# Optimization experiments

Measured on AMD Instinct MI355X. Metric: run time of the kernel, lower is better.

Reference implementation:

```python
import jax, jax.numpy as jnp
import numpy as np

NUM_HEADS = 16

def setup_inputs() -> dict:
    key = jax.random.key(0)
    k1, k2, k3, k4 = jax.random.split(key, 4)
    B, N, C = 4, 2048, 1024
    x = jax.random.normal(k1, (B, N, C), dtype=jnp.float32)
    xpos = jax.random.randint(k2, (B, N), 0, 2048, dtype=jnp.int64)
    Wqkv = jax.random.normal(k3, (C, 3 * C), dtype=jnp.float32) * (C ** -0.5)
    Wproj = jax.random.normal(k4, (C, C), dtype=jnp.float32) * (C ** -0.5)
    bproj = jnp.zeros((C,), dtype=jnp.float32)
    return {"x": x, "xpos": xpos, "Wqkv": Wqkv, "Wproj": Wproj, "bproj": bproj}

def reference(x, xpos, Wqkv, Wproj, bproj):
    # rope is None in this configuration, so xpos is unused (matches torch default path).
    B, N, C = x.shape
    H = NUM_HEADS
    Dh = C // H
    scale = Dh ** -0.5
    qkv = jnp.einsum('bnc,cd->bnd', x, Wqkv)              # [B, N, 3C]
    qkv = qkv.reshape(B, N, 3, H, Dh)
    q, k, v = qkv[:, :, 0], qkv[:, :, 1], qkv[:, :, 2]    # [B, N, H, Dh]
    scores = jnp.einsum('bnhd,bmhd->bhnm', q, k) * scale  # [B, H, N, N]
    attn = jax.nn.softmax(scores, axis=-1)
    out = jnp.einsum('bhnm,bmhd->bnhd', attn, v)          # [B, N, H, Dh]
    out = out.reshape(B, N, C)
    return jnp.einsum('bnc,cd->bnd', out, Wproj) + bproj
```

## Files before the change

kernel.cpp:

```cpp
#include <hip/hip_runtime.h>
#include <stdint.h>

#define DEVINL __device__ __forceinline__

typedef __bf16 bf16x8 __attribute__((ext_vector_type(8)));
typedef float f32x4 __attribute__((ext_vector_type(4)));
typedef float f32x16 __attribute__((ext_vector_type(16)));
typedef uint32_t u32x4 __attribute__((ext_vector_type(4)));

DEVINL uint16_t f2bf(float f) {
    uint32_t u = __builtin_bit_cast(uint32_t, f);
    uint32_t r = (u + 0x7FFFu + ((u >> 16) & 1u)) >> 16;
    return (uint16_t)r;
}

DEVINL bf16x8 ld8(const uint16_t* p) {
    u32x4 v = *(const u32x4*)p;
    return __builtin_bit_cast(bf16x8, v);
}

DEVINL void gload16(const void* g, void* l) {
    __builtin_amdgcn_global_load_lds(
        (const __attribute__((address_space(1))) uint32_t*)g,
        (__attribute__((address_space(3))) uint32_t*)l, 16, 0, 0);
}

DEVINL uint32_t cvtpk(float lo, float hi) {
    uint32_t r;
    asm("v_cvt_pk_bf16_f32 %0, %1, %2" : "=v"(r) : "v"(lo), "v"(hi));
    return r;
}

DEVINL float exp2_fast(float x) {
    float r;
    asm("v_exp_f32 %0, %1" : "=v"(r) : "v"(x));
    return r;
}

DEVINL void transW_body(const float* __restrict__ W, uint16_t* __restrict__ WT,
                        int Nn, int n0, int k0, int tid, uint16_t* t) {
#pragma unroll
    for (int i = 0; i < 4; ++i) {
        int c = tid + i * 256;
        int kr = c >> 4, nc = c & 15;
        float4 v = *(const float4*)(W + (size_t)(k0 + kr) * Nn + n0 + nc * 4);
        t[(nc * 4 + 0) * 65 + kr] = f2bf(v.x);
        t[(nc * 4 + 1) * 65 + kr] = f2bf(v.y);
        t[(nc * 4 + 2) * 65 + kr] = f2bf(v.z);
        t[(nc * 4 + 3) * 65 + kr] = f2bf(v.w);
    }
    __syncthreads();
#pragma unroll
    for (int i = 0; i < 2; ++i) {
        int c = tid + i * 256;
        int nr = c >> 3, kc = c & 7;
        union { uint16_t u[8]; u32x4 v; } o;
#pragma unroll
        for (int j = 0; j < 8; ++j) o.u[j] = t[nr * 65 + kc * 8 + j];
        *(u32x4*)(WT + (size_t)(n0 + nr) * 1024 + k0 + kc * 8) = o.v;
    }
}

__global__ void k_prep(const float* __restrict__ x, uint16_t* __restrict__ xb,
                       const float* __restrict__ Wqkv, uint16_t* __restrict__ wqkvT,
                       const float* __restrict__ Wproj, uint16_t* __restrict__ wprojT) {
    __shared__ uint16_t t[64 * 65];
    int bid = blockIdx.x;
    int tid = threadIdx.x;
    if (bid < 4096) {
        int i = bid * 256 + tid;
        const float4* src = (const float4*)x + (size_t)i * 2;
        float4 a = src[0], b = src[1];
        union { uint16_t u[8]; u32x4 v; } o;
        o.u[0] = f2bf(a.x); o.u[1] = f2bf(a.y); o.u[2] = f2bf(a.z); o.u[3] = f2bf(a.w);
        o.u[4] = f2bf(b.x); o.u[5] = f2bf(b.y); o.u[6] = f2bf(b.z); o.u[7] = f2bf(b.w);
        ((u32x4*)xb)[i] = o.v;
    } else if (bid < 4864) {
        int idx = bid - 4096;
        transW_body(Wqkv, wqkvT, 3072, (idx % 48) * 64, (idx / 48) * 64, tid, t);
    } else {
        int idx = bid - 4864;
        transW_body(Wproj, wprojT, 1024, (idx % 16) * 64, (idx / 16) * 64, tid, t);
    }
}

template <int MODE>
__global__ __launch_bounds__(256) void k_gemm(
    const uint16_t* __restrict__ A, const uint16_t* __restrict__ BT,
    const float* __restrict__ bias,
    uint16_t* __restrict__ qo, uint16_t* __restrict__ ko, uint16_t* __restrict__ vo,
    float* __restrict__ out) {
    __shared__ uint16_t smem[16640];
    uint16_t* a_lds = smem;
    uint16_t* b_lds = smem + 8192;
    int tid = threadIdx.x;
    int w = tid >> 6, l = tid & 63;
    int l15 = l & 15, l4 = l >> 4;
    int bid = blockIdx.x;
    int mt = ((bid & 7) << 3) + ((bid >> 3) & 7);
    int nt = bid >> 6;
    int m0 = mt * 128, n0 = nt * 128;
    int wr = w >> 1, wc = w & 1;
    f32x4 acc[4][4] = {};

    for (int kt = 0; kt < 16; ++kt) {
#pragma unroll
        for (int i = 0; i < 4; ++i) {
            int c = i * 256 + w * 64 + l;
            int row = c >> 3, slot = c & 7;
            int kc = slot ^ (row & 7);
            gload16(A + (size_t)(m0 + row) * 1024 + kt * 64 + kc * 8,
                    a_lds + (size_t)(i * 256 + w * 64) * 8);
            gload16(BT + (size_t)(n0 + row) * 1024 + kt * 64 + kc * 8,
                    b_lds + (size_t)(i * 256 + w * 64) * 8);
        }
        __syncthreads();
#pragma unroll
        for (int kkk = 0; kkk < 2; ++kkk) {
            bf16x8 af[4], bfr[4];
#pragma unroll
            for (int i = 0; i < 4; ++i) {
                int row = wr * 64 + i * 16 + l15;
                af[i] = ld8(a_lds + row * 64 + ((kkk * 4 + l4) ^ (row & 7)) * 8);
                int rowb = wc * 64 + i * 16 + l15;
                bfr[i] = ld8(b_lds + rowb * 64 + ((kkk * 4 + l4) ^ (rowb & 7)) * 8);
            }
#pragma unroll
            for (int i = 0; i < 4; ++i)
#pragma unroll
                for (int j = 0; j < 4; ++j)
                    acc[i][j] = __builtin_amdgcn_mfma_f32_16x16x32_bf16(
                        af[i], bfr[j], acc[i][j], 0, 0, 0);
        }
        __syncthreads();
    }

    if constexpr (MODE == 0) {
        if (n0 >= 2048) {
#pragma unroll
            for (int i = 0; i < 4; ++i)
#pragma unroll
                for (int j = 0; j < 4; ++j) {
                    int dl = wc * 64 + j * 16 + l15;
                    int ml = wr * 64 + i * 16 + l4 * 4;
                    union { uint16_t u[4]; uint2 v2; } pk;
#pragma unroll
                    for (int r = 0; r < 4; ++r) pk.u[r] = f2bf(acc[i][j][r]);
                    *(uint2*)&smem[dl * 130 + ml] = pk.v2;
                }
            __syncthreads();
            int b = m0 >> 11, nbase = m0 & 2047;
#pragma unroll
            for (int pass = 0; pass < 8; ++pass) {
                int dl = pass * 16 + (tid >> 4);
                int mloc = (tid & 15) * 8;
                u32x4 val = *(u32x4*)&smem[dl * 130 + mloc];
                int d = n0 + dl;
                int h = (d >> 6) & 15, dh = d & 63;
                *(u32x4*)(vo + ((size_t)(b * 16 + h) * 64 + dh) * 2048 + nbase + mloc) = val;
            }
        } else {
#pragma unroll
            for (int i = 0; i < 4; ++i)
#pragma unroll
                for (int j = 0; j < 4; ++j) {
                    int d = n0 + wc * 64 + j * 16 + l15;
                    int s = d >> 10, h = (d >> 6) & 15, dh = d & 63;
                    uint16_t* dst0 = (s == 0) ? qo : ko;
                    float sc = (s == 0) ? 0.18033688011112042f : 1.0f;
#pragma unroll
                    for (int r = 0; r < 4; ++r) {
                        int m = m0 + wr * 64 + i * 16 + l4 * 4 + r;
                        int b = m >> 11, n = m & 2047;
                        dst0[((size_t)(b * 16 + h) * 2048 + n) * 64 + dh] = f2bf(acc[i][j][r] * sc);
                    }
                }
        }
    } else {
#pragma unroll
        for (int j = 0; j < 4; ++j) {
            int d = n0 + wc * 64 + j * 16 + l15;
            float bv = bias[d];
#pragma unroll
            for (int i = 0; i < 4; ++i)
#pragma unroll
                for (int r = 0; r < 4; ++r) {
                    int m = m0 + wr * 64 + i * 16 + l4 * 4 + r;
                    out[(size_t)m * 1024 + d] = acc[i][j][r] + bv;
                }
        }
    }
}

__global__ __launch_bounds__(256) void k_attn(
    const uint16_t* __restrict__ q, const uint16_t* __restrict__ kk_,
    const uint16_t* __restrict__ vt, uint16_t* __restrict__ o) {
    __shared__ uint16_t k_lds[2][64 * 64];
    __shared__ uint16_t v_lds[2][64 * 64];
    int tid = threadIdx.x;
    int w = tid >> 6, l = tid & 63;
    int l31 = l & 31, g = l >> 5;
    int bid = blockIdx.x;
    int slot = bid >> 3;
    int bh = (bid & 7) * 8 + (slot >> 4);
    int qt = slot & 15;
    int qrow = qt * 128 + w * 32 + l31;
    const uint16_t* qb = q + ((size_t)bh * 2048 + qrow) * 64;
    const uint16_t* kbase = kk_ + (size_t)bh * 2048 * 64;
    const uint16_t* vbase = vt + (size_t)bh * 64 * 2048;

    bf16x8 qf[4];
#pragma unroll
    for (int kv = 0; kv < 4; ++kv) qf[kv] = ld8(qb + kv * 16 + g * 8);

    int c0 = w * 128 + l;
    int rr0 = c0 >> 3, sl0 = c0 & 7;
    int kc0 = sl0 ^ (rr0 & 7);
    int rr1 = rr0 + 8, kc1 = sl0 ^ (rr1 & 7);
    const uint16_t* kp0 = kbase + rr0 * 64 + kc0 * 8;
    const uint16_t* kp1 = kbase + rr1 * 64 + kc1 * 8;
    const uint16_t* vp0 = vbase + (size_t)rr0 * 2048 + kc0 * 8;
    const uint16_t* vp1 = vbase + (size_t)rr1 * 2048 + kc1 * 8;
    uint16_t* kd0 = k_lds[0] + w * 1024;
    uint16_t* kd1 = k_lds[1] + w * 1024;
    uint16_t* vd0 = v_lds[0] + w * 1024;
    uint16_t* vd1 = v_lds[1] + w * 1024;

    f32x16 oa[2] = {};
    float lsum = 0.f;

    auto stage = [&](uint16_t* kd, uint16_t* vd) {
        gload16(kp0, kd);       gload16(kp1, kd + 512);
        gload16(vp0, vd);       gload16(vp1, vd + 512);
        kp0 += 4096; kp1 += 4096; vp0 += 64; vp1 += 64;
    };

    stage(kd0, vd0);

    auto body = [&](int t, const uint16_t* kb, const uint16_t* vb,
                    uint16_t* kdn, uint16_t* vdn) {
        asm volatile("s_waitcnt vmcnt(2)\n\ts_barrier" ::: "memory");
        if (t < 31) stage(kdn, vdn);

        bf16x8 pfrag[4];
#pragma unroll
        for (int j = 0; j < 2; ++j) {
            int key = j * 32 + l31;
            f32x16 stj = {};
            __builtin_amdgcn_s_setprio(1);
#pragma unroll
            for (int kv = 0; kv < 4; ++kv) {
                bf16x8 kf = ld8(kb + key * 64 + ((2 * kv + g) ^ (key & 7)) * 8);
                stj = __builtin_amdgcn_mfma_f32_32x32x16_bf16(kf, qf[kv], stj, 0, 0, 0);
            }
            __builtin_amdgcn_s_setprio(0);
#pragma unroll
            for (int h = 0; h < 2; ++h) {
                float e[8];
#pragma unroll
                for (int jj = 0; jj < 8; ++jj) e[jj] = exp2_fast(stj[h * 8 + jj]);
                lsum += ((e[0] + e[1]) + (e[2] + e[3])) + ((e[4] + e[5]) + (e[6] + e[7]));
                uint32_t a0 = cvtpk(e[0], e[1]), a1 = cvtpk(e[2], e[3]);
                uint32_t b0 = cvtpk(e[4], e[5]), b1 = cvtpk(e[6], e[7]);
                auto r0 = __builtin_amdgcn_permlane32_swap(a0, b0, false, false);
                auto r1 = __builtin_amdgcn_permlane32_swap(a1, b1, false, false);
                u32x4 f;
                f[0] = r0[0]; f[1] = r1[0]; f[2] = r0[1]; f[3] = r1[1];
                pfrag[j * 2 + h] = __builtin_bit_cast(bf16x8, f);
            }
        }

        if (t < 31) asm volatile("s_waitcnt vmcnt(4)\n\ts_barrier" ::: "memory");
        else        asm volatile("s_waitcnt vmcnt(0)\n\ts_barrier" ::: "memory");

        __builtin_amdgcn_s_setprio(1);
#pragma unroll
        for (int kv = 0; kv < 4; ++kv) {
#pragma unroll
            for (int dt = 0; dt < 2; ++dt) {
                int dh = dt * 32 + l31;
                bf16x8 vf = ld8(vb + dh * 64 + ((2 * kv + g) ^ (dh & 7)) * 8);
                oa[dt] = __builtin_amdgcn_mfma_f32_32x32x16_bf16(vf, pfrag[kv], oa[dt], 0, 0, 0);
            }
        }
        __builtin_amdgcn_s_setprio(0);
    };

    for (int kt = 0; kt < 32; kt += 2) {
        body(kt,     k_lds[0], v_lds[0], kd1, vd1);
        body(kt + 1, k_lds[1], v_lds[1], kd0, vd0);
    }

    float ltot = lsum + __shfl_xor(lsum, 32, 64);
    float inv = 1.0f / ltot;
    int b = bh >> 4, h = bh & 15;
    uint16_t* ob = o + ((size_t)(b * 2048 + qrow)) * 1024 + h * 64;
#pragma unroll
    for (int dt = 0; dt < 2; ++dt)
#pragma unroll
        for (int rq = 0; rq < 4; ++rq) {
            union { uint16_t u[4]; uint2 v; } pk;
#pragma unroll
            for (int rr = 0; rr < 4; ++rr) pk.u[rr] = f2bf(oa[dt][rq * 4 + rr] * inv);
            int dh0 = dt * 32 + rq * 8 + g * 4;
            *(uint2*)(ob + dh0) = pk.v;
        }
}

extern "C" void kernel_launch(void* const* d_in, const int* in_sizes, int n_in,
                              void* d_out, int out_size, void* d_ws, size_t ws_size,
                              hipStream_t stream) {
    const float* x     = (const float*)d_in[0];
    const float* Wqkv  = (const float*)d_in[2];
    const float* Wproj = (const float*)d_in[3];
    const float* bproj = (const float*)d_in[4];
    float* out = (float*)d_out;

    char* ws = (char*)d_ws;
    uint16_t* xb     = (uint16_t*)(ws);
    uint16_t* wqkvT  = (uint16_t*)(ws + 16777216);
    uint16_t* wprojT = (uint16_t*)(ws + 23068672);
    uint16_t* qws    = (uint16_t*)(ws + 25165824);
    uint16_t* kws    = (uint16_t*)(ws + 41943040);
    uint16_t* vT     = (uint16_t*)(ws + 58720256);
    uint16_t* attnout = xb;

    k_prep<<<dim3(5120), dim3(256), 0, stream>>>(x, xb, Wqkv, wqkvT, Wproj, wprojT);
    k_gemm<0><<<dim3(1536), dim3(256), 0, stream>>>(xb, wqkvT, nullptr, qws, kws, vT, nullptr);
    k_attn<<<dim3(1024), dim3(256), 0, stream>>>(qws, kws, vT, attnout);
    k_gemm<1><<<dim3(512), dim3(256), 0, stream>>>(attnout, wprojT, bproj, nullptr, nullptr, nullptr, out);
}
```

Measured before the change: 204.4 us.

## Restructure GEMM to 256x128 tiles, 512 threads, double-buffered LDS pipeline

Rewrites the bf16 GEMM kernel to use 256x128 output tiles with 8 waves, double-buffered LDS staging through global_load_lds so the next K-slice loads while the current one computes, and s_setprio around the MFMA bursts. Grid sizes are halved and 96KB of dynamic LDS is requested. The aim is to hide global load latency and raise arithmetic intensity per block. In exchange, the large LDS footprint and 512-thread blocks reduce occupancy, and the 256-block projection GEMM may underfill the GPU's compute units.

```diff
diff --git a/kernel.cpp b/kernel.cpp
--- a/kernel.cpp
+++ b/kernel.cpp
@@ -85,108 +85,124 @@
 }
 
 template <int MODE>
-__global__ __launch_bounds__(256) void k_gemm(
+__global__ __launch_bounds__(512) void k_gemm(
     const uint16_t* __restrict__ A, const uint16_t* __restrict__ BT,
     const float* __restrict__ bias,
     uint16_t* __restrict__ qo, uint16_t* __restrict__ ko, uint16_t* __restrict__ vo,
     float* __restrict__ out) {
-    __shared__ uint16_t smem[16640];
-    uint16_t* a_lds = smem;
-    uint16_t* b_lds = smem + 8192;
+    extern __shared__ uint16_t lds[];
     int tid = threadIdx.x;
     int w = tid >> 6, l = tid & 63;
     int l15 = l & 15, l4 = l >> 4;
+    int wr = w >> 2, wc = w & 3;
     int bid = blockIdx.x;
-    int mt = ((bid & 7) << 3) + ((bid >> 3) & 7);
-    int nt = bid >> 6;
-    int m0 = mt * 128, n0 = nt * 128;
-    int wr = w >> 1, wc = w & 1;
-    f32x4 acc[4][4] = {};
-
-    for (int kt = 0; kt < 16; ++kt) {
-#pragma unroll
-        for (int i = 0; i < 4; ++i) {
-            int c = i * 256 + w * 64 + l;
-            int row = c >> 3, slot = c & 7;
-            int kc = slot ^ (row & 7);
-            gload16(A + (size_t)(m0 + row) * 1024 + kt * 64 + kc * 8,
-                    a_lds + (size_t)(i * 256 + w * 64) * 8);
-            gload16(BT + (size_t)(n0 + row) * 1024 + kt * 64 + kc * 8,
-                    b_lds + (size_t)(i * 256 + w * 64) * 8);
-        }
+    int mt = (bid & 7) * 4 + ((bid >> 3) & 3);
+    int nt = bid >> 5;
+    int m0 = mt * 256, n0 = nt * 128;
+
+    int r0 = tid >> 3, sl0 = tid & 7;
+    int kc = sl0 ^ (r0 & 7);
+    const uint16_t* pA = A + (size_t)(m0 + r0) * 1024 + kc * 8;
+    const uint16_t* pB = BT + (size_t)(n0 + r0) * 1024 + kc * 8;
+    int wofs = w * 512;
+
+    f32x4 acc[8][2] = {};
+
+    auto stageK = [&](int ks, int abA, int abB) {
+#pragma unroll
+        for (int q = 0; q < 4; ++q)
+            gload16(pA + q * 65536 + ks * 64, lds + abA + q * 4096 + wofs);
+#pragma unroll
+        for (int li = 0; li < 2; ++li)
+            gload16(pB + li * 65536 + ks * 64, lds + abB + li * 4096 + wofs);
+    };
+
+    auto computeK = [&](int abA, int abB) {
+        const uint16_t* Ah = lds + abA + wr * 8192;
+        const uint16_t* Bb = lds + abB;
+#pragma unroll
+        for (int kk = 0; kk < 2; ++kk) {
+            int ch = ((kk * 4 + l4) ^ (l15 & 7)) * 8;
+            bf16x8 af[8], bf[2];
+#pragma unroll
+            for (int fi = 0; fi < 8; ++fi)
+                af[fi] = ld8(Ah + (fi * 16 + l15) * 64 + ch);
+#pragma unroll
+            for (int fj = 0; fj < 2; ++fj)
+                bf[fj] = ld8(Bb + (wc * 32 + fj * 16 + l15) * 64 + ch);
+            __builtin_amdgcn_s_setprio(1);
+#pragma unroll
+            for (int fi = 0; fi < 8; ++fi)
+#pragma unroll
+                for (int fj = 0; fj < 2; ++fj)
+                    acc[fi][fj] = __builtin_amdgcn_mfma_f32_16x16x32_bf16(
+                        af[fi], bf[fj], acc[fi][fj], 0, 0, 0);
+            __builtin_amdgcn_s_setprio(0);
+        }
+    };
+
+    stageK(0, 0, 32768);
+    asm volatile("s_waitcnt vmcnt(0)\n\ts_barrier" ::: "memory");
+    for (int s = 0; s < 16; s += 2) {
+        if (s + 1 < 16) stageK(s + 1, 16384, 40960);
+        computeK(0, 32768);
+        asm volatile("s_waitcnt vmcnt(0)\n\ts_barrier" ::: "memory");
+        if (s + 2 < 16) stageK(s + 2, 0, 32768);
+        computeK(16384, 40960);
+        asm volatile("s_waitcnt vmcnt(0)\n\ts_barrier" ::: "memory");
+    }
+
+    if constexpr (MODE == 0) {
+        int b = m0 >> 11, nbase = m0 & 2047;
+        if (n0 >= 2048) {
+#pragma unroll
+            for (int fi = 0; fi < 8; ++fi)
+#pragma unroll
+                for (int fj = 0; fj < 2; ++fj) {
+                    int dl = wc * 32 + fj * 16 + l15;
+                    int ml = wr * 128 + fi * 16 + l4 * 4;
+                    union { uint16_t u[4]; uint2 v2; } pk;
+#pragma unroll
+                    for (int r = 0; r < 4; ++r) pk.u[r] = f2bf(acc[fi][fj][r]);
+                    *(uint2*)&lds[dl * 264 + ml] = pk.v2;
+                }
         __syncthreads();
 #pragma unroll
-        for (int kkk = 0; kkk < 2; ++kkk) {
-            bf16x8 af[4], bfr[4];
-#pragma unroll
-            for (int i = 0; i < 4; ++i) {
-                int row = wr * 64 + i * 16 + l15;
-                af[i] = ld8(a_lds + row * 64 + ((kkk * 4 + l4) ^ (row & 7)) * 8);
-                int rowb = wc * 64 + i * 16 + l15;
-                bfr[i] = ld8(b_lds + rowb * 64 + ((kkk * 4 + l4) ^ (rowb & 7)) * 8);
-            }
-#pragma unroll
-            for (int i = 0; i < 4; ++i)
-#pragma unroll
-                for (int j = 0; j < 4; ++j)
-                    acc[i][j] = __builtin_amdgcn_mfma_f32_16x16x32_bf16(
-                        af[i], bfr[j], acc[i][j], 0, 0, 0);
-        }
-        __syncthreads();
-    }
-
-    if constexpr (MODE == 0) {
-        if (n0 >= 2048) {
-#pragma unroll
-            for (int i = 0; i < 4; ++i)
-#pragma unroll
-                for (int j = 0; j < 4; ++j) {
-                    int dl = wc * 64 + j * 16 + l15;
-                    int ml = wr * 64 + i * 16 + l4 * 4;
-                    union { uint16_t u[4]; uint2 v2; } pk;
-#pragma unroll
-                    for (int r = 0; r < 4; ++r) pk.u[r] = f2bf(acc[i][j][r]);
-                    *(uint2*)&smem[dl * 130 + ml] = pk.v2;
-                }
-            __syncthreads();
-            int b = m0 >> 11, nbase = m0 & 2047;
-#pragma unroll
-            for (int pass = 0; pass < 8; ++pass) {
-                int dl = pass * 16 + (tid >> 4);
-                int mloc = (tid & 15) * 8;
-                u32x4 val = *(u32x4*)&smem[dl * 130 + mloc];
-                int d = n0 + dl;
-                int h = (d >> 6) & 15, dh = d & 63;
-                *(u32x4*)(vo + ((size_t)(b * 16 + h) * 64 + dh) * 2048 + nbase + mloc) = val;
+            for (int it = 0; it < 8; ++it) {
+                int idx = it * 512 + tid;
+                int row = idx >> 5, col = (idx & 31) * 8;
+                u32x4 val = *(u32x4*)&lds[row * 264 + col];
+                int dv = (n0 - 2048) + row;
+                int h = dv >> 6, dh = dv & 63;
+                *(u32x4*)(vo + ((size_t)(b * 16 + h) * 64 + dh) * 2048 + nbase + col) = val;
             }
         } else {
-#pragma unroll
-            for (int i = 0; i < 4; ++i)
-#pragma unroll
-                for (int j = 0; j < 4; ++j) {
-                    int d = n0 + wc * 64 + j * 16 + l15;
-                    int s = d >> 10, h = (d >> 6) & 15, dh = d & 63;
-                    uint16_t* dst0 = (s == 0) ? qo : ko;
-                    float sc = (s == 0) ? 0.18033688011112042f : 1.0f;
+            float sc = (n0 < 1024) ? 0.18033688011112042f : 1.0f;
+            uint16_t* dst0 = (n0 < 1024) ? qo : ko;
+#pragma unroll
+            for (int fi = 0; fi < 8; ++fi)
+#pragma unroll
+                for (int fj = 0; fj < 2; ++fj) {
+                    int d = n0 + wc * 32 + fj * 16 + l15;
+                    int h = (d >> 6) & 15, dh = d & 63;
 #pragma unroll
                     for (int r = 0; r < 4; ++r) {
-                        int m = m0 + wr * 64 + i * 16 + l4 * 4 + r;
-                        int b = m >> 11, n = m & 2047;
-                        dst0[((size_t)(b * 16 + h) * 2048 + n) * 64 + dh] = f2bf(acc[i][j][r] * sc);
+                        int n = nbase + wr * 128 + fi * 16 + l4 * 4 + r;
+                        dst0[((size_t)(b * 16 + h) * 2048 + n) * 64 + dh] = f2bf(acc[fi][fj][r] * sc);
                     }
                 }
         }
     } else {
 #pragma unroll
-        for (int j = 0; j < 4; ++j) {
-            int d = n0 + wc * 64 + j * 16 + l15;
+        for (int fj = 0; fj < 2; ++fj) {
+            int d = n0 + wc * 32 + fj * 16 + l15;
             float bv = bias[d];
 #pragma unroll
-            for (int i = 0; i < 4; ++i)
+            for (int fi = 0; fi < 8; ++fi)
 #pragma unroll
                 for (int r = 0; r < 4; ++r) {
-                    int m = m0 + wr * 64 + i * 16 + l4 * 4 + r;
-                    out[(size_t)m * 1024 + d] = acc[i][j][r] + bv;
+                    int m = m0 + wr * 128 + fi * 16 + l4 * 4 + r;
+                    out[(size_t)m * 1024 + d] = acc[fi][fj][r] + bv;
                 }
         }
     }
@@ -326,7 +342,7 @@
     uint16_t* attnout = xb;
 
     k_prep<<<dim3(5120), dim3(256), 0, stream>>>(x, xb, Wqkv, wqkvT, Wproj, wprojT);
-    k_gemm<0><<<dim3(1536), dim3(256), 0, stream>>>(xb, wqkvT, nullptr, qws, kws, vT, nullptr);
+    k_gemm<0><<<dim3(768), dim3(512), 98304, stream>>>(xb, wqkvT, nullptr, qws, kws, vT, nullptr);
     k_attn<<<dim3(1024), dim3(256), 0, stream>>>(qws, kws, vT, attnout);
-    k_gemm<1><<<dim3(512), dim3(256), 0, stream>>>(attnout, wprojT, bproj, nullptr, nullptr, nullptr, out);
-}
+    k_gemm<1><<<dim3(256), dim3(512), 98304, stream>>>(attnout, wprojT, bproj, nullptr, nullptr, nullptr, out);
+}
```

New measurement: 195.9 us. -4.1%, faster.
